# Kernel optimization log

Measured on AMD Instinct MI355X. Metric: run time of the kernel, lower is better.

## Reference

```python
import jax, jax.numpy as jnp
import numpy as np

EPS_LN = 1e-5

def layer_norm(x, g, b):
    mu = x.mean(-1, keepdims=True)
    var = ((x - mu) ** 2).mean(-1, keepdims=True)
    return (x - mu) / jnp.sqrt(var + EPS_LN) * g + b

def spike(x):
    # MultiSpike: quantized spike activation, forward = clip(round(x), 0, 4)
    return jnp.clip(jnp.round(x), 0.0, 4.0)

def setup_inputs() -> dict:
    key = jax.random.key(0)
    ks = jax.random.split(key, 8)
    B, C, H, W = 16, 256, 56, 56
    hid = 128
    inp = {}
    inp['feature_map'] = jax.random.normal(ks[0], (B, C, H, W), jnp.float32)
    inp['audio_feature'] = jax.random.normal(ks[1], (B, 1, C), jnp.float32)
    # MINE params
    inp['w1'] = jax.random.normal(ks[2], (hid, 2 * C), jnp.float32) / np.sqrt(2 * C)
    inp['b1'] = jnp.zeros((hid,), jnp.float32)
    inp['g1'] = jnp.ones((hid,), jnp.float32)
    inp['beta1'] = jnp.zeros((hid,), jnp.float32)
    inp['w2'] = jax.random.normal(ks[3], (hid // 2, hid), jnp.float32) / np.sqrt(hid)
    inp['b2'] = jnp.zeros((hid // 2,), jnp.float32)
    inp['g2'] = jnp.ones((hid // 2,), jnp.float32)
    inp['beta2'] = jnp.zeros((hid // 2,), jnp.float32)
    inp['w3'] = jax.random.normal(ks[4], (1, hid // 2), jnp.float32) / np.sqrt(hid // 2)
    inp['b3'] = jnp.zeros((1,), jnp.float32)
    # MI params
    inp['pw'] = jax.random.normal(ks[5], (C, C), jnp.float32) / np.sqrt(C)
    inp['pb'] = jnp.zeros((C,), jnp.float32)
    inp['pg'] = jnp.ones((C,), jnp.float32)
    inp['pbeta'] = jnp.zeros((C,), jnp.float32)
    return inp

def reference(feature_map, audio_feature, w1, b1, g1, beta1, w2, b2, g2, beta2,
              w3, b3, pw, pb, pg, pbeta):
    B, C, H, W = feature_map.shape
    # visual tokens: [B*H*W, C]
    visual = feature_map.transpose(0, 2, 3, 1).reshape(B * H * W, C)
    # broadcast audio to every spatial position: [B*H*W, C]
    audio = jnp.broadcast_to(audio_feature[:, 0][:, None, None, :], (B, H, W, C)).reshape(B * H * W, C)
    # MINE MLP on joint features
    joint = jnp.concatenate([visual, audio], axis=1)            # [BHW, 2C]
    h = spike(layer_norm(joint @ w1.T + b1, g1, beta1))          # [BHW, 128]
    h = spike(layer_norm(h @ w2.T + b2, g2, beta2))              # [BHW, 64]
    mi = (h @ w3.T + b3)[:, 0]                                   # [BHW]
    mi_map = mi.reshape(B, 1, H * W)
    fm_flat = feature_map.reshape(B, C, H * W)
    # MI-weighted pooling: [B,1,C]
    x = jnp.einsum('bos,bcs->boc', mi_map, fm_flat)
    x = x @ pw.T + pb                                            # proj (dropout = eval identity)
    x = spike(layer_norm(x, pg, pbeta))                          # [B,1,C]
    fusion_map = jnp.einsum('bchw,bc->bchw', feature_map, x[:, 0])
    mi4 = mi_map.reshape(B, 1, H, W)
    mi4 = (mi4 - mi4.min()) / (mi4.max() - mi4.min() + 1e-6)     # global min-max norm
    return fusion_map, mi4
```

## Files before the change

kernel.cpp:

```cpp
#include <hip/hip_runtime.h>

#define HW 3136
#define NPOS 12845056

__device__ __forceinline__ unsigned fkey(float f) {
  unsigned u = __float_as_uint(f);
  return (u & 0x80000000u) ? ~u : (u | 0x80000000u);
}
__device__ __forceinline__ float funkey(unsigned u) {
  return __uint_as_float((u & 0x80000000u) ? (u & 0x7FFFFFFFu) : ~u);
}
__device__ __forceinline__ float spikef(float x) {
  return fminf(fmaxf(rintf(x), 0.0f), 4.0f);
}

__global__ __launch_bounds__(256) void prep_kernel(
    const float* __restrict__ audio, const float* __restrict__ w1,
    const float* __restrict__ b1, const float* __restrict__ w2,
    float* __restrict__ a_pre, float* __restrict__ w1t,
    float* __restrict__ w2t, float* __restrict__ pool,
    unsigned* __restrict__ mm)
{
  __shared__ float au[256];
  const int bx = blockIdx.x, t = threadIdx.x;
  if (bx < 128) {
    int idx = bx * 256 + t;
    int c = idx >> 7, j = idx & 127;
    w1t[idx] = w1[j * 512 + c];
  } else if (bx < 160) {
    int idx = (bx - 128) * 256 + t;
    int k = idx >> 6, j2 = idx & 63;
    w2t[idx] = w2[j2 * 128 + k];
  } else if (bx < 176) {
    int b = bx - 160;
    au[t] = audio[b * 256 + t];
    __syncthreads();
    int w = t >> 6, l = t & 63;
    float a0 = au[l], a1 = au[l + 64], a2 = au[l + 128], a3 = au[l + 192];
    for (int jj = 0; jj < 32; ++jj) {
      int j = w * 32 + jj;
      const float* row = w1 + j * 512 + 256;
      float s = row[l] * a0 + row[l + 64] * a1 + row[l + 128] * a2 + row[l + 192] * a3;
      #pragma unroll
      for (int off = 32; off; off >>= 1) s += __shfl_xor(s, off);
      if (l == 0) a_pre[b * 128 + j] = s + b1[j];
    }
  } else {
    for (int i = t; i < 4096; i += 256) pool[i] = 0.0f;
    if (t == 0) { mm[0] = 0xFFFFFFFFu; mm[1] = 0u; }
  }
}

__global__ __launch_bounds__(512, 6) void mlp_kernel(
    const float* __restrict__ fm, const float* __restrict__ w1t,
    const float* __restrict__ w2t, const float* __restrict__ b2,
    const float* __restrict__ w3, const float* __restrict__ b3,
    const float* __restrict__ g1, const float* __restrict__ be1,
    const float* __restrict__ g2, const float* __restrict__ be2,
    const float* __restrict__ a_pre, float* __restrict__ mi_out,
    float* __restrict__ pool, unsigned* __restrict__ mm)
{
  __shared__ __align__(16) float smem[12288];
  __shared__ float red[16][64];
  __shared__ float miL[64];

  const int b  = blockIdx.y;
  const int s0 = blockIdx.x * 64;
  const int t  = threadIdx.x;
  const int l  = t & 63;
  const int wv = __builtin_amdgcn_readfirstlane(t >> 6);

  const float* fmblk = fm + (size_t)b * 256 * HW + s0;
  float* const h1f = smem;

  auto stage = [&](int ch, int bd) {
    {
      const float* g = fmblk + (size_t)(ch * 32 + wv * 4 + (l >> 4)) * HW
                       + (l & 15) * 4;
      float* d = smem + bd * 2048 + wv * 256;
      __builtin_amdgcn_global_load_lds(
          (const __attribute__((address_space(1))) void*)g,
          (__attribute__((address_space(3))) void*)d, 16, 0, 0);
    }
    #pragma unroll
    for (int i = 0; i < 2; ++i) {
      const float* g = w1t + (size_t)(ch * 32 + wv * 4 + i * 2 + (l >> 5)) * 128
                       + (l & 31) * 4;
      float* d = smem + 4096 + bd * 4096 + (wv * 4 + i * 2) * 128;
      __builtin_amdgcn_global_load_lds(
          (const __attribute__((address_space(1))) void*)g,
          (__attribute__((address_space(3))) void*)d, 16, 0, 0);
    }
  };

  float acc[16];
  #pragma unroll
  for (int j = 0; j < 16; ++j) acc[j] = 0.f;

  stage(0, 0);
  __syncthreads();
  #pragma unroll 1
  for (int ch = 0; ch < 8; ++ch) {
    if (ch < 7) stage(ch + 1, (ch + 1) & 1);
    const float* Ab = smem + (ch & 1) * 2048;
    const float* Bb = smem + 4096 + (ch & 1) * 4096 + wv * 16;
    #pragma unroll 4
    for (int k = 0; k < 32; ++k) {
      float x = Ab[k * 64 + l];
      const float* wk = Bb + k * 128;
      float4 q0 = *(const float4*)(wk);
      float4 q1 = *(const float4*)(wk + 4);
      float4 q2 = *(const float4*)(wk + 8);
      float4 q3 = *(const float4*)(wk + 12);
      acc[ 0] = fmaf(x, q0.x, acc[ 0]); acc[ 1] = fmaf(x, q0.y, acc[ 1]);
      acc[ 2] = fmaf(x, q0.z, acc[ 2]); acc[ 3] = fmaf(x, q0.w, acc[ 3]);
      acc[ 4] = fmaf(x, q1.x, acc[ 4]); acc[ 5] = fmaf(x, q1.y, acc[ 5]);
      acc[ 6] = fmaf(x, q1.z, acc[ 6]); acc[ 7] = fmaf(x, q1.w, acc[ 7]);
      acc[ 8] = fmaf(x, q2.x, acc[ 8]); acc[ 9] = fmaf(x, q2.y, acc[ 9]);
      acc[10] = fmaf(x, q2.z, acc[10]); acc[11] = fmaf(x, q2.w, acc[11]);
      acc[12] = fmaf(x, q3.x, acc[12]); acc[13] = fmaf(x, q3.y, acc[13]);
      acc[14] = fmaf(x, q3.z, acc[14]); acc[15] = fmaf(x, q3.w, acc[15]);
    }
    __syncthreads();
  }
  {
    const float4* ap = (const float4*)(a_pre + b * 128 + wv * 16);
    #pragma unroll
    for (int q = 0; q < 4; ++q) {
      float4 a4 = ap[q];
      acc[4*q+0] += a4.x; acc[4*q+1] += a4.y;
      acc[4*q+2] += a4.z; acc[4*q+3] += a4.w;
    }
  }

  float mu, inv;
  {
    float s = 0.f;
    #pragma unroll
    for (int j = 0; j < 16; ++j) s += acc[j];
    red[wv][l] = s;
    __syncthreads();
    s = 0.f;
    #pragma unroll
    for (int q = 0; q < 8; ++q) s += red[q][l];
    mu = s * (1.0f/128.0f);
    float s2 = 0.f;
    #pragma unroll
    for (int j = 0; j < 16; ++j) { float d = acc[j] - mu; s2 = fmaf(d, d, s2); }
    red[8 + wv][l] = s2;
    __syncthreads();
    s2 = 0.f;
    #pragma unroll
    for (int q = 0; q < 8; ++q) s2 += red[8 + q][l];
    inv = 1.0f / sqrtf(s2 * (1.0f/128.0f) + 1e-5f);
  }

  {
    const float* gp = g1  + wv * 16;
    const float* bp = be1 + wv * 16;
    #pragma unroll
    for (int j = 0; j < 16; ++j) {
      float h = spikef((acc[j] - mu) * inv * gp[j] + bp[j]);
      h1f[(wv * 16 + j) * 64 + l] = h;
    }
  }
  __syncthreads();

  float a2[8];
  #pragma unroll
  for (int p = 0; p < 8; ++p) a2[p] = 0.f;
  {
    const float* hrow = h1f + wv * 8;
    const float* w2p  = w2t + l;
    #pragma unroll 2
    for (int k2 = 0; k2 < 128; ++k2) {
      float wval = w2p[k2 * 64];
      const float* hk = hrow + k2 * 64;
      float4 x0 = *(const float4*)(hk);
      float4 x1 = *(const float4*)(hk + 4);
      a2[0] = fmaf(x0.x, wval, a2[0]); a2[1] = fmaf(x0.y, wval, a2[1]);
      a2[2] = fmaf(x0.z, wval, a2[2]); a2[3] = fmaf(x0.w, wval, a2[3]);
      a2[4] = fmaf(x1.x, wval, a2[4]); a2[5] = fmaf(x1.y, wval, a2[5]);
      a2[6] = fmaf(x1.z, wval, a2[6]); a2[7] = fmaf(x1.w, wval, a2[7]);
    }
  }
  {
    const float b2l = b2[l];
    #pragma unroll
    for (int p = 0; p < 8; ++p) a2[p] += b2l;
  }

  float miv[8];
  {
    const float g2l = g2[l], be2l = be2[l], w3l = w3[l];
    const float b3v = b3[0];
    #pragma unroll
    for (int p = 0; p < 8; ++p) {
      float s = a2[p];
      #pragma unroll
      for (int off = 32; off; off >>= 1) s += __shfl_xor(s, off);
      float mu2 = s * (1.0f/64.0f);
      float d = a2[p] - mu2;
      float s2 = d * d;
      #pragma unroll
      for (int off = 32; off; off >>= 1) s2 += __shfl_xor(s2, off);
      float inv2 = 1.0f / sqrtf(s2 * (1.0f/64.0f) + 1e-5f);
      float sp = spikef(d * inv2 * g2l + be2l) * w3l;
      #pragma unroll
      for (int off = 32; off; off >>= 1) sp += __shfl_xor(sp, off);
      miv[p] = sp + b3v;
    }
  }

  {
    float m = miv[0];
    #pragma unroll
    for (int p = 1; p < 8; ++p) m = (l == p) ? miv[p] : m;
    if (l < 8) {
      mi_out[b * HW + s0 + wv * 8 + l] = m;
      miL[wv * 8 + l] = m;
    }
  }
  __syncthreads();

  if (wv == 0) {
    float v = miL[l];
    float mn = v, mx = v;
    #pragma unroll
    for (int off = 32; off; off >>= 1) {
      mn = fminf(mn, __shfl_xor(mn, off));
      mx = fmaxf(mx, __shfl_xor(mx, off));
    }
    if (l == 0) {
      unsigned kmn = fkey(mn), kmx = fkey(mx);
      volatile unsigned* vmm = (volatile unsigned*)mm;
      if (kmn < vmm[0]) atomicMin(&mm[0], kmn);
      if (kmx > vmm[1]) atomicMax(&mm[1], kmx);
    }
  }

  {
    const float mval = miL[l];
    const float* fp2 = fmblk + l + (size_t)(wv << 5) * HW;
    #pragma unroll 4
    for (int ci = 0; ci < 32; ++ci) {
      float v = fp2[(size_t)ci * HW] * mval;
      #pragma unroll
      for (int off = 32; off; off >>= 1) v += __shfl_xor(v, off);
      if (l == 0) atomicAdd(&pool[b * 256 + (wv << 5) + ci], v);
    }
  }
}

__global__ __launch_bounds__(256) void scale_kernel(
    const float* __restrict__ pool, const float* __restrict__ pw,
    const float* __restrict__ pb, const float* __restrict__ pg,
    const float* __restrict__ pbeta, float* __restrict__ scale,
    const unsigned* __restrict__ mm, float* __restrict__ gpar)
{
  __shared__ float pl[256];
  __shared__ float xsh[256];
  __shared__ float rs[4], rs2[4];
  int b = blockIdx.x, t = threadIdx.x;
  pl[t] = pool[b*256 + t];
  __syncthreads();
  int w = t >> 6, l = t & 63;
  float p0 = pl[l], p1 = pl[l+64], p2 = pl[l+128], p3 = pl[l+192];
  for (int jj = 0; jj < 64; ++jj) {
    int j = w*64 + jj;
    const float* row = pw + j*256;
    float s = row[l]*p0 + row[l+64]*p1 + row[l+128]*p2 + row[l+192]*p3;
    #pragma unroll
    for (int off = 32; off; off >>= 1) s += __shfl_xor(s, off);
    if (l == 0) xsh[j] = s;
  }
  __syncthreads();
  float x = xsh[t] + pb[t];
  float s = x;
  #pragma unroll
  for (int off = 32; off; off >>= 1) s += __shfl_xor(s, off);
  if (l == 0) rs[w] = s;
  __syncthreads();
  float mu = (rs[0]+rs[1]+rs[2]+rs[3]) * (1.0f/256.0f);
  float d = x - mu;
  float s2 = d*d;
  #pragma unroll
  for (int off = 32; off; off >>= 1) s2 += __shfl_xor(s2, off);
  if (l == 0) rs2[w] = s2;
  __syncthreads();
  float var = (rs2[0]+rs2[1]+rs2[2]+rs2[3]) * (1.0f/256.0f);
  float v = d / sqrtf(var + 1e-5f) * pg[t] + pbeta[t];
  scale[b*256 + t] = spikef(v);
  if (b == 0 && t == 0) {
    float mn = funkey(mm[0]), mx = funkey(mm[1]);
    gpar[0] = mn;
    gpar[1] = mx - mn + 1e-6f;
  }
}

__global__ __launch_bounds__(256) void fuse_kernel(
    const float4* __restrict__ fm4, const float* __restrict__ scale,
    const float4* __restrict__ mi4, const float* __restrict__ gpar,
    float4* __restrict__ out4, float4* __restrict__ mi4out)
{
  const int c = blockIdx.x, b = blockIdx.y, t = threadIdx.x;
  if (c < 256) {
    float s = scale[b * 256 + c];
    size_t base = ((size_t)b * 256 + c) * 784;
    #pragma unroll
    for (int i = 0; i < 3; ++i) {
      int idx = t + i * 256;
      float4 v = fm4[base + idx];
      out4[base + idx] = make_float4(v.x*s, v.y*s, v.z*s, v.w*s);
    }
    int idx = t + 768;
    if (idx < 784) {
      float4 v = fm4[base + idx];
      out4[base + idx] = make_float4(v.x*s, v.y*s, v.z*s, v.w*s);
    }
  } else {
    float gmin = gpar[0], den = gpar[1];
    size_t base = (size_t)b * 784;
    #pragma unroll
    for (int i = 0; i < 3; ++i) {
      int idx = t + i * 256;
      float4 v = mi4[base + idx];
      mi4out[base + idx] = make_float4((v.x-gmin)/den, (v.y-gmin)/den,
                                       (v.z-gmin)/den, (v.w-gmin)/den);
    }
    int idx = t + 768;
    if (idx < 784) {
      float4 v = mi4[base + idx];
      mi4out[base + idx] = make_float4((v.x-gmin)/den, (v.y-gmin)/den,
                                       (v.z-gmin)/den, (v.w-gmin)/den);
    }
  }
}

extern "C" void kernel_launch(void* const* d_in, const int* in_sizes, int n_in,
                              void* d_out, int out_size, void* d_ws, size_t ws_size,
                              hipStream_t stream)
{
  const float* fm    = (const float*)d_in[0];
  const float* audio = (const float*)d_in[1];
  const float* w1    = (const float*)d_in[2];
  const float* b1    = (const float*)d_in[3];
  const float* g1    = (const float*)d_in[4];
  const float* be1   = (const float*)d_in[5];
  const float* w2    = (const float*)d_in[6];
  const float* b2    = (const float*)d_in[7];
  const float* g2    = (const float*)d_in[8];
  const float* be2   = (const float*)d_in[9];
  const float* w3    = (const float*)d_in[10];
  const float* b3    = (const float*)d_in[11];
  const float* pw    = (const float*)d_in[12];
  const float* pb    = (const float*)d_in[13];
  const float* pg    = (const float*)d_in[14];
  const float* pbeta = (const float*)d_in[15];

  float* ws    = (float*)d_ws;
  float* a_pre = ws;
  float* pool  = ws + 2048;
  float* scale = ws + 6144;
  float* mi    = ws + 10240;
  float* w1t   = ws + 60416;
  float* w2t   = ws + 93184;
  unsigned* mm = (unsigned*)(ws + 101376);
  float* gpar  = ws + 101378;

  float* out    = (float*)d_out;
  float* mi4out = out + NPOS;

  prep_kernel<<<177, 256, 0, stream>>>(audio, w1, b1, w2, a_pre, w1t, w2t,
                                       pool, mm);
  mlp_kernel<<<dim3(49, 16), 512, 0, stream>>>(fm, w1t, w2t, b2, w3, b3,
                                               g1, be1, g2, be2,
                                               a_pre, mi, pool, mm);
  scale_kernel<<<16, 256, 0, stream>>>(pool, pw, pb, pg, pbeta, scale, mm, gpar);
  fuse_kernel<<<dim3(257, 16), 256, 0, stream>>>((const float4*)fm, scale,
                                                 (const float4*)mi, gpar,
                                                 (float4*)out, (float4*)mi4out);
}
```

Measured before the change: 331.4 us.

## Register-tile first MLP GEMM 8x8 with split-K reduction and readlane second layer

Restructures the first-layer GEMM so each thread computes an 8x8 register tile (positions × hidden units). Waves split K four ways and reduce their partial sums through shared memory, which raises FMA-per-LDS-load reuse. The second layer now holds w2 columns in registers and broadcasts them with readlane, and the per-position layernorm reductions are reorganised to go across waves via shared memory. Occupancy hint drops from 6 to 4 to fit the 64 accumulators, at the cost of extra syncs and lower occupancy.

```diff
diff --git a/kernel.cpp b/kernel.cpp
--- a/kernel.cpp
+++ b/kernel.cpp
@@ -12,6 +12,9 @@
 }
 __device__ __forceinline__ float spikef(float x) {
   return fminf(fmaxf(rintf(x), 0.0f), 4.0f);
+}
+__device__ __forceinline__ float rdlane(float v, int src) {
+  return __int_as_float(__builtin_amdgcn_readlane(__float_as_int(v), src));
 }
 
 __global__ __launch_bounds__(256) void prep_kernel(
@@ -51,7 +54,7 @@
   }
 }
 
-__global__ __launch_bounds__(512, 6) void mlp_kernel(
+__global__ __launch_bounds__(512, 4) void mlp_kernel(
     const float* __restrict__ fm, const float* __restrict__ w1t,
     const float* __restrict__ w2t, const float* __restrict__ b2,
     const float* __restrict__ w3, const float* __restrict__ b3,
@@ -62,16 +65,18 @@
 {
   __shared__ __align__(16) float smem[12288];
   __shared__ float red[16][64];
-  __shared__ float miL[64];
 
   const int b  = blockIdx.y;
   const int s0 = blockIdx.x * 64;
   const int t  = threadIdx.x;
   const int l  = t & 63;
   const int wv = __builtin_amdgcn_readfirstlane(t >> 6);
+  const int jw = wv & 1;
+  const int kq = wv >> 1;
+  const int p8 = l >> 3;
+  const int j8 = l & 7;
 
   const float* fmblk = fm + (size_t)b * 256 * HW + s0;
-  float* const h1f = smem;
 
   auto stage = [&](int ch, int bd) {
     {
@@ -93,139 +98,235 @@
     }
   };
 
-  float acc[16];
+  float acc[8][8];
   #pragma unroll
-  for (int j = 0; j < 16; ++j) acc[j] = 0.f;
+  for (int ii = 0; ii < 8; ++ii)
+    #pragma unroll
+    for (int jj = 0; jj < 8; ++jj) acc[ii][jj] = 0.f;
 
   stage(0, 0);
   __syncthreads();
   #pragma unroll 1
   for (int ch = 0; ch < 8; ++ch) {
     if (ch < 7) stage(ch + 1, (ch + 1) & 1);
-    const float* Ab = smem + (ch & 1) * 2048;
-    const float* Bb = smem + 4096 + (ch & 1) * 4096 + wv * 16;
-    #pragma unroll 4
-    for (int k = 0; k < 32; ++k) {
-      float x = Ab[k * 64 + l];
-      const float* wk = Bb + k * 128;
-      float4 q0 = *(const float4*)(wk);
-      float4 q1 = *(const float4*)(wk + 4);
-      float4 q2 = *(const float4*)(wk + 8);
-      float4 q3 = *(const float4*)(wk + 12);
-      acc[ 0] = fmaf(x, q0.x, acc[ 0]); acc[ 1] = fmaf(x, q0.y, acc[ 1]);
-      acc[ 2] = fmaf(x, q0.z, acc[ 2]); acc[ 3] = fmaf(x, q0.w, acc[ 3]);
-      acc[ 4] = fmaf(x, q1.x, acc[ 4]); acc[ 5] = fmaf(x, q1.y, acc[ 5]);
-      acc[ 6] = fmaf(x, q1.z, acc[ 6]); acc[ 7] = fmaf(x, q1.w, acc[ 7]);
-      acc[ 8] = fmaf(x, q2.x, acc[ 8]); acc[ 9] = fmaf(x, q2.y, acc[ 9]);
-      acc[10] = fmaf(x, q2.z, acc[10]); acc[11] = fmaf(x, q2.w, acc[11]);
-      acc[12] = fmaf(x, q3.x, acc[12]); acc[13] = fmaf(x, q3.y, acc[13]);
-      acc[14] = fmaf(x, q3.z, acc[14]); acc[15] = fmaf(x, q3.w, acc[15]);
+    const float* Ab = smem + (ch & 1) * 2048 + kq * 8 * 64 + p8 * 8;
+    const float* Bb = smem + 4096 + (ch & 1) * 4096 + kq * 8 * 128 + jw * 64 + j8 * 8;
+    #pragma unroll
+    for (int k = 0; k < 8; ++k) {
+      float4 a0 = *(const float4*)(Ab + k * 64);
+      float4 a1 = *(const float4*)(Ab + k * 64 + 4);
+      float4 b0 = *(const float4*)(Bb + k * 128);
+      float4 b1 = *(const float4*)(Bb + k * 128 + 4);
+      float av[8] = {a0.x, a0.y, a0.z, a0.w, a1.x, a1.y, a1.z, a1.w};
+      float bv[8] = {b0.x, b0.y, b0.z, b0.w, b1.x, b1.y, b1.z, b1.w};
+      #pragma unroll
+      for (int ii = 0; ii < 8; ++ii)
+        #pragma unroll
+        for (int jj = 0; jj < 8; ++jj)
+          acc[ii][jj] = fmaf(av[ii], bv[jj], acc[ii][jj]);
     }
     __syncthreads();
   }
-  {
-    const float4* ap = (const float4*)(a_pre + b * 128 + wv * 16);
-    #pragma unroll
-    for (int q = 0; q < 4; ++q) {
-      float4 a4 = ap[q];
-      acc[4*q+0] += a4.x; acc[4*q+1] += a4.y;
-      acc[4*q+2] += a4.z; acc[4*q+3] += a4.w;
-    }
-  }
-
-  float mu, inv;
-  {
-    float s = 0.f;
-    #pragma unroll
-    for (int j = 0; j < 16; ++j) s += acc[j];
-    red[wv][l] = s;
-    __syncthreads();
-    s = 0.f;
-    #pragma unroll
-    for (int q = 0; q < 8; ++q) s += red[q][l];
-    mu = s * (1.0f/128.0f);
-    float s2 = 0.f;
-    #pragma unroll
-    for (int j = 0; j < 16; ++j) { float d = acc[j] - mu; s2 = fmaf(d, d, s2); }
-    red[8 + wv][l] = s2;
-    __syncthreads();
-    s2 = 0.f;
-    #pragma unroll
-    for (int q = 0; q < 8; ++q) s2 += red[8 + q][l];
-    inv = 1.0f / sqrtf(s2 * (1.0f/128.0f) + 1e-5f);
-  }
-
-  {
-    const float* gp = g1  + wv * 16;
-    const float* bp = be1 + wv * 16;
-    #pragma unroll
-    for (int j = 0; j < 16; ++j) {
-      float h = spikef((acc[j] - mu) * inv * gp[j] + bp[j]);
-      h1f[(wv * 16 + j) * 64 + l] = h;
+
+  float4 xw0, xw1, xw2, xw3;
+  {
+    const float* wp = w2t + (2 * l) * 64 + wv * 8;
+    xw0 = *(const float4*)(wp);
+    xw1 = *(const float4*)(wp + 4);
+    xw2 = *(const float4*)(wp + 64);
+    xw3 = *(const float4*)(wp + 68);
+  }
+
+  float* scr = smem;
+  auto wr = [&]() {
+    float* p = scr + jw * 4096 + l * 2;
+    #pragma unroll
+    for (int ii = 0; ii < 8; ++ii)
+      #pragma unroll
+      for (int q = 0; q < 4; ++q)
+        *(float2*)(p + (ii * 4 + q) * 128) = make_float2(acc[ii][2*q], acc[ii][2*q+1]);
+  };
+  auto ad = [&]() {
+    const float* p = scr + jw * 4096 + l * 2;
+    #pragma unroll
+    for (int ii = 0; ii < 8; ++ii)
+      #pragma unroll
+      for (int q = 0; q < 4; ++q) {
+        float2 v = *(const float2*)(p + (ii * 4 + q) * 128);
+        acc[ii][2*q] += v.x; acc[ii][2*q+1] += v.y;
+      }
+  };
+  if (kq == 1) wr();
+  __syncthreads();
+  if (kq == 0) ad();
+  __syncthreads();
+  if (kq == 3) wr();
+  __syncthreads();
+  if (kq == 2) ad();
+  __syncthreads();
+  if (kq == 2) wr();
+  __syncthreads();
+  if (kq == 0) ad();
+
+  float mu[8], inv[8];
+  if (kq == 0) {
+    const float* ap = a_pre + b * 128 + jw * 64 + j8 * 8;
+    float4 A0 = *(const float4*)(ap), A1 = *(const float4*)(ap + 4);
+    float av[8] = {A0.x, A0.y, A0.z, A0.w, A1.x, A1.y, A1.z, A1.w};
+    float s[8];
+    #pragma unroll
+    for (int ii = 0; ii < 8; ++ii) {
+      float v = 0.f;
+      #pragma unroll
+      for (int jj = 0; jj < 8; ++jj) { acc[ii][jj] += av[jj]; v += acc[ii][jj]; }
+      v += __shfl_xor(v, 1); v += __shfl_xor(v, 2); v += __shfl_xor(v, 4);
+      s[ii] = v;
+    }
+    if (j8 == 0) {
+      *(float4*)&red[jw][p8 * 8]     = make_float4(s[0], s[1], s[2], s[3]);
+      *(float4*)&red[jw][p8 * 8 + 4] = make_float4(s[4], s[5], s[6], s[7]);
+    }
+  }
+  __syncthreads();
+  if (kq == 0) {
+    float4 r00 = *(const float4*)&red[0][p8 * 8];
+    float4 r01 = *(const float4*)&red[0][p8 * 8 + 4];
+    float4 r10 = *(const float4*)&red[1][p8 * 8];
+    float4 r11 = *(const float4*)&red[1][p8 * 8 + 4];
+    mu[0] = (r00.x + r10.x) * (1.0f/128.0f); mu[1] = (r00.y + r10.y) * (1.0f/128.0f);
+    mu[2] = (r00.z + r10.z) * (1.0f/128.0f); mu[3] = (r00.w + r10.w) * (1.0f/128.0f);
+    mu[4] = (r01.x + r11.x) * (1.0f/128.0f); mu[5] = (r01.y + r11.y) * (1.0f/128.0f);
+    mu[6] = (r01.z + r11.z) * (1.0f/128.0f); mu[7] = (r01.w + r11.w) * (1.0f/128.0f);
+    float s[8];
+    #pragma unroll
+    for (int ii = 0; ii < 8; ++ii) {
+      float v = 0.f;
+      #pragma unroll
+      for (int jj = 0; jj < 8; ++jj) { float d = acc[ii][jj] - mu[ii]; v = fmaf(d, d, v); }
+      v += __shfl_xor(v, 1); v += __shfl_xor(v, 2); v += __shfl_xor(v, 4);
+      s[ii] = v;
+    }
+    if (j8 == 0) {
+      *(float4*)&red[2 + jw][p8 * 8]     = make_float4(s[0], s[1], s[2], s[3]);
+      *(float4*)&red[2 + jw][p8 * 8 + 4] = make_float4(s[4], s[5], s[6], s[7]);
+    }
+  }
+  __syncthreads();
+  if (kq == 0) {
+    float4 v00 = *(const float4*)&red[2][p8 * 8];
+    float4 v01 = *(const float4*)&red[2][p8 * 8 + 4];
+    float4 v10 = *(const float4*)&red[3][p8 * 8];
+    float4 v11 = *(const float4*)&red[3][p8 * 8 + 4];
+    inv[0] = 1.0f / sqrtf((v00.x + v10.x) * (1.0f/128.0f) + 1e-5f);
+    inv[1] = 1.0f / sqrtf((v00.y + v10.y) * (1.0f/128.0f) + 1e-5f);
+    inv[2] = 1.0f / sqrtf((v00.z + v10.z) * (1.0f/128.0f) + 1e-5f);
+    inv[3] = 1.0f / sqrtf((v00.w + v10.w) * (1.0f/128.0f) + 1e-5f);
+    inv[4] = 1.0f / sqrtf((v01.x + v11.x) * (1.0f/128.0f) + 1e-5f);
+    inv[5] = 1.0f / sqrtf((v01.y + v11.y) * (1.0f/128.0f) + 1e-5f);
+    inv[6] = 1.0f / sqrtf((v01.z + v11.z) * (1.0f/128.0f) + 1e-5f);
+    inv[7] = 1.0f / sqrtf((v01.w + v11.w) * (1.0f/128.0f) + 1e-5f);
+    const float* gp = g1  + jw * 64 + j8 * 8;
+    const float* bp = be1 + jw * 64 + j8 * 8;
+    float4 G0 = *(const float4*)(gp), G1 = *(const float4*)(gp + 4);
+    float4 B0 = *(const float4*)(bp), B1 = *(const float4*)(bp + 4);
+    float gv[8] = {G0.x, G0.y, G0.z, G0.w, G1.x, G1.y, G1.z, G1.w};
+    float bv[8] = {B0.x, B0.y, B0.z, B0.w, B1.x, B1.y, B1.z, B1.w};
+    #pragma unroll
+    for (int jj = 0; jj < 8; ++jj) {
+      float4 h0, h1v;
+      h0.x  = spikef((acc[0][jj] - mu[0]) * inv[0] * gv[jj] + bv[jj]);
+      h0.y  = spikef((acc[1][jj] - mu[1]) * inv[1] * gv[jj] + bv[jj]);
+      h0.z  = spikef((acc[2][jj] - mu[2]) * inv[2] * gv[jj] + bv[jj]);
+      h0.w  = spikef((acc[3][jj] - mu[3]) * inv[3] * gv[jj] + bv[jj]);
+      h1v.x = spikef((acc[4][jj] - mu[4]) * inv[4] * gv[jj] + bv[jj]);
+      h1v.y = spikef((acc[5][jj] - mu[5]) * inv[5] * gv[jj] + bv[jj]);
+      h1v.z = spikef((acc[6][jj] - mu[6]) * inv[6] * gv[jj] + bv[jj]);
+      h1v.w = spikef((acc[7][jj] - mu[7]) * inv[7] * gv[jj] + bv[jj]);
+      float* hp = smem + (jw * 64 + j8 * 8 + jj) * 64 + p8 * 8;
+      *(float4*)(hp) = h0;
+      *(float4*)(hp + 4) = h1v;
     }
   }
   __syncthreads();
 
   float a2[8];
   #pragma unroll
-  for (int p = 0; p < 8; ++p) a2[p] = 0.f;
-  {
-    const float* hrow = h1f + wv * 8;
-    const float* w2p  = w2t + l;
-    #pragma unroll 2
-    for (int k2 = 0; k2 < 128; ++k2) {
-      float wval = w2p[k2 * 64];
-      const float* hk = hrow + k2 * 64;
-      float4 x0 = *(const float4*)(hk);
-      float4 x1 = *(const float4*)(hk + 4);
-      a2[0] = fmaf(x0.x, wval, a2[0]); a2[1] = fmaf(x0.y, wval, a2[1]);
-      a2[2] = fmaf(x0.z, wval, a2[2]); a2[3] = fmaf(x0.w, wval, a2[3]);
-      a2[4] = fmaf(x1.x, wval, a2[4]); a2[5] = fmaf(x1.y, wval, a2[5]);
-      a2[6] = fmaf(x1.z, wval, a2[6]); a2[7] = fmaf(x1.w, wval, a2[7]);
-    }
-  }
-  {
-    const float b2l = b2[l];
-    #pragma unroll
-    for (int p = 0; p < 8; ++p) a2[p] += b2l;
-  }
-
-  float miv[8];
-  {
-    const float g2l = g2[l], be2l = be2[l], w3l = w3[l];
-    const float b3v = b3[0];
-    #pragma unroll
-    for (int p = 0; p < 8; ++p) {
-      float s = a2[p];
-      #pragma unroll
-      for (int off = 32; off; off >>= 1) s += __shfl_xor(s, off);
-      float mu2 = s * (1.0f/64.0f);
-      float d = a2[p] - mu2;
-      float s2 = d * d;
-      #pragma unroll
-      for (int off = 32; off; off >>= 1) s2 += __shfl_xor(s2, off);
-      float inv2 = 1.0f / sqrtf(s2 * (1.0f/64.0f) + 1e-5f);
-      float sp = spikef(d * inv2 * g2l + be2l) * w3l;
-      #pragma unroll
-      for (int off = 32; off; off >>= 1) sp += __shfl_xor(sp, off);
-      miv[p] = sp + b3v;
-    }
-  }
-
-  {
-    float m = miv[0];
-    #pragma unroll
-    for (int p = 1; p < 8; ++p) m = (l == p) ? miv[p] : m;
-    if (l < 8) {
-      mi_out[b * HW + s0 + wv * 8 + l] = m;
-      miL[wv * 8 + l] = m;
-    }
-  }
-  __syncthreads();
+  for (int j = 0; j < 8; ++j) a2[j] = 0.f;
+  {
+    const float* hp = smem + l;
+    #pragma unroll 4
+    for (int m = 0; m < 64; ++m) {
+      float he = hp[(2 * m) * 64];
+      float ho = hp[(2 * m + 1) * 64];
+      a2[0] = fmaf(ho, rdlane(xw2.x, m), fmaf(he, rdlane(xw0.x, m), a2[0]));
+      a2[1] = fmaf(ho, rdlane(xw2.y, m), fmaf(he, rdlane(xw0.y, m), a2[1]));
+      a2[2] = fmaf(ho, rdlane(xw2.z, m), fmaf(he, rdlane(xw0.z, m), a2[2]));
+      a2[3] = fmaf(ho, rdlane(xw2.w, m), fmaf(he, rdlane(xw0.w, m), a2[3]));
+      a2[4] = fmaf(ho, rdlane(xw3.x, m), fmaf(he, rdlane(xw1.x, m), a2[4]));
+      a2[5] = fmaf(ho, rdlane(xw3.y, m), fmaf(he, rdlane(xw1.y, m), a2[5]));
+      a2[6] = fmaf(ho, rdlane(xw3.z, m), fmaf(he, rdlane(xw1.z, m), a2[6]));
+      a2[7] = fmaf(ho, rdlane(xw3.w, m), fmaf(he, rdlane(xw1.w, m), a2[7]));
+    }
+  }
+  {
+    float4 b20 = *(const float4*)(b2 + wv * 8);
+    float4 b21 = *(const float4*)(b2 + wv * 8 + 4);
+    a2[0] += b20.x; a2[1] += b20.y; a2[2] += b20.z; a2[3] += b20.w;
+    a2[4] += b21.x; a2[5] += b21.y; a2[6] += b21.z; a2[7] += b21.w;
+  }
+
+  {
+    float s = 0.f;
+    #pragma unroll
+    for (int j = 0; j < 8; ++j) s += a2[j];
+    red[wv][l] = s;
+  }
+  __syncthreads();
+  float mu2;
+  {
+    float s = 0.f;
+    #pragma unroll
+    for (int q = 0; q < 8; ++q) s += red[q][l];
+    mu2 = s * (1.0f/64.0f);
+    float s2 = 0.f;
+    #pragma unroll
+    for (int j = 0; j < 8; ++j) { float d = a2[j] - mu2; s2 = fmaf(d, d, s2); }
+    red[8 + wv][l] = s2;
+  }
+  __syncthreads();
+  float mip;
+  {
+    float s2 = 0.f;
+    #pragma unroll
+    for (int q = 0; q < 8; ++q) s2 += red[8 + q][l];
+    float inv2 = 1.0f / sqrtf(s2 * (1.0f/64.0f) + 1e-5f);
+    float4 g20 = *(const float4*)(g2 + wv * 8);
+    float4 g21 = *(const float4*)(g2 + wv * 8 + 4);
+    float4 e20 = *(const float4*)(be2 + wv * 8);
+    float4 e21 = *(const float4*)(be2 + wv * 8 + 4);
+    float4 w30 = *(const float4*)(w3 + wv * 8);
+    float4 w31 = *(const float4*)(w3 + wv * 8 + 4);
+    float gv[8] = {g20.x, g20.y, g20.z, g20.w, g21.x, g21.y, g21.z, g21.w};
+    float ev[8] = {e20.x, e20.y, e20.z, e20.w, e21.x, e21.y, e21.z, e21.w};
+    float wv3[8] = {w30.x, w30.y, w30.z, w30.w, w31.x, w31.y, w31.z, w31.w};
+    float p = 0.f;
+    #pragma unroll
+    for (int j = 0; j < 8; ++j) {
+      float sp = spikef((a2[j] - mu2) * inv2 * gv[j] + ev[j]);
+      p = fmaf(sp, wv3[j], p);
+    }
+    mip = p;
+  }
+  __syncthreads();
+  red[wv][l] = mip;
+  __syncthreads();
+  float mi = b3[0];
+  #pragma unroll
+  for (int q = 0; q < 8; ++q) mi += red[q][l];
 
   if (wv == 0) {
-    float v = miL[l];
-    float mn = v, mx = v;
+    mi_out[b * HW + s0 + l] = mi;
+    float mn = mi, mx = mi;
     #pragma unroll
     for (int off = 32; off; off >>= 1) {
       mn = fminf(mn, __shfl_xor(mn, off));
@@ -240,11 +341,10 @@
   }
 
   {
-    const float mval = miL[l];
     const float* fp2 = fmblk + l + (size_t)(wv << 5) * HW;
     #pragma unroll 4
     for (int ci = 0; ci < 32; ++ci) {
-      float v = fp2[(size_t)ci * HW] * mval;
+      float v = fp2[(size_t)ci * HW] * mi;
       #pragma unroll
       for (int off = 32; off; off >>= 1) v += __shfl_xor(v, off);
       if (l == 0) atomicAdd(&pool[b * 256 + (wv << 5) + ci], v);
```

After: 333.3 us. About the same (+0.6%).
